# Kernel optimization log

Hardware: AMD Instinct MI355X
Metric: run time of the kernel (lower is better)

Reference implementation:

```python
import jax, jax.numpy as jnp
import numpy as np

NHID = 256
NHEADS = 8
HEAD_F = NHID // NHEADS  # GAT per-head out_features
ALPHA = 0.1              # GAT LeakyReLU slope
NEG = -9e15


def _leaky(x, slope):
    return jnp.where(x >= 0, x, slope * x)


def _cnorm(x, axis):
    # matches Norm.compute_norm: (x - mean) / (std_unbiased + 1e-6)
    m = jnp.mean(x, axis=axis, keepdims=True)
    s = jnp.std(x, axis=axis, keepdims=True, ddof=1)
    return (x - m) / (s + 1e-6)


def _norm(x):
    # Norm('bn') forward: per-sample normalize over features (dim=1 of x[i]) then nodes (dim=0)
    return _cnorm(_cnorm(x, axis=2), axis=1)


def setup_inputs() -> dict:
    key = jax.random.key(0)
    ks = jax.random.split(key, 12)
    B, N, E, H, D = 4, 1024, NHID, NHEADS, HEAD_F

    def xavier(k, shape, gain=1.414):
        fan_in, fan_out = shape[-2], shape[-1]
        a = gain * np.sqrt(6.0 / (fan_in + fan_out))
        return jax.random.uniform(k, shape, jnp.float32, -a, a)

    return {
        "x": jax.random.normal(ks[0], (B, N, E), jnp.float32),
        "src": jax.random.normal(ks[1], (N, B, E), jnp.float32),
        "adj": jax.random.randint(ks[2], (B, N, N), 0, 2, jnp.int32),
        "Wg": xavier(ks[3], (H, E, D)),                 # per-head GAT W
        "a1": xavier(ks[4], (H, D, 1))[..., 0],         # a[:D]
        "a2": xavier(ks[5], (H, D, 1))[..., 0],         # a[D:]
        "lin_w": xavier(ks[6], (E, E), gain=1.0),
        "lin_b": jnp.zeros((E,), jnp.float32),
        "in_proj_w": xavier(ks[7], (3 * E, E), gain=1.0),
        "in_proj_b": jnp.zeros((3 * E,), jnp.float32),
        "out_proj_w": xavier(ks[8], (E, E), gain=1.0),
        "out_proj_b": jnp.zeros((E,), jnp.float32),
    }


def reference(x, src, adj, Wg, a1, a2, lin_w, lin_b, in_proj_w, in_proj_b, out_proj_w, out_proj_b):
    B, N, E = x.shape
    H, D = NHEADS, HEAD_F

    # --- multi-head dense GAT (all heads vectorized) ---
    Wh = jnp.einsum("bnf,hfd->hbnd", x, Wg)                      # [H,B,N,D]
    s1 = jnp.einsum("hbnd,hd->hbn", Wh, a1)                      # a1 . Wh_i
    s2 = jnp.einsum("hbnd,hd->hbn", Wh, a2)                      # a2 . Wh_j
    e = _leaky(s1[..., :, None] + s2[..., None, :], ALPHA)       # [H,B,N,N]
    e = jnp.where(adj[None] > 0, e, NEG)
    attn = jax.nn.softmax(e, axis=-1)                            # [H,B,N,N]
    hp = _leaky(jnp.einsum("hbnm,hbmd->hbnd", attn, Wh), 0.01)   # F.leaky_relu default

    x = x + jnp.transpose(hp, (1, 2, 0, 3)).reshape(B, N, H * D)
    e_out = jnp.mean(attn, axis=0)                               # [B,N,N]

    # --- norm1 -> linear -> norm2 ---
    x = _norm(x) @ lin_w.T + lin_b
    x = _norm(x)

    # --- nn.MultiheadAttention(query=x, key=x, value=src) ---
    srcb = jnp.transpose(src, (1, 0, 2))                         # [B,N,E]
    Wq, Wk, Wv = in_proj_w[:E], in_proj_w[E:2 * E], in_proj_w[2 * E:]
    bq, bk, bv = in_proj_b[:E], in_proj_b[E:2 * E], in_proj_b[2 * E:]
    Dh = E // H
    q = (x @ Wq.T + bq).reshape(B, N, H, Dh)
    k = (x @ Wk.T + bk).reshape(B, N, H, Dh)
    v = (srcb @ Wv.T + bv).reshape(B, N, H, Dh)
    scores = jnp.einsum("bqhd,bkhd->bhqk", q, k) / jnp.sqrt(jnp.float32(Dh))
    p = jax.nn.softmax(scores, axis=-1)
    o = jnp.einsum("bhqk,bkhd->bqhd", p, v).reshape(B, N, E)
    x = o @ out_proj_w.T + out_proj_b                            # [B,N,E]

    return (x, e_out)
```

## Files before the change

### kernel.cpp

```cpp
#include <hip/hip_runtime.h>
#include <hip/hip_bf16.h>

#define BIAS_OFF 196608
#define S1_OFF   198400
#define S2_OFF   231168
#define CS_OFF   263936
#define ST1_OFF  296704
#define ST2_OFF  298752
#define A_OFF    300800
#define MX_OFF   825088
#define RS_OFF   857856
#define PK_OFF   890624
#define B_OFF    1349376
#define C_OFF    2397952
#define FLAG_F   3446528

#define NEGC (-9.0e15f)

typedef __attribute__((ext_vector_type(8))) short bf16x8s;
typedef __attribute__((ext_vector_type(4))) float f32x4;

static __device__ __forceinline__ float bf2f(unsigned short u) {
  union { unsigned int i; float f; } v; v.i = ((unsigned int)u) << 16; return v.f;
}
static __device__ __forceinline__ unsigned short f2bf(float f) {
  union { float f; unsigned int u; } v; v.f = f;
  unsigned int r = (v.u + 0x7FFFu + ((v.u >> 16) & 1u)) >> 16;
  return (unsigned short)r;
}
static __device__ __forceinline__ float ldin(const void* p, long i, int bf) {
  return bf ? bf2f(((const unsigned short*)p)[i]) : ((const float*)p)[i];
}
static __device__ __forceinline__ unsigned short rdbf(const void* p, long i, int bf) {
  if (bf) return ((const unsigned short*)p)[i];
  return f2bf(((const float*)p)[i]);
}
static __device__ __forceinline__ void stout(void* p, long i, float v, int bf) {
  if (bf) ((unsigned short*)p)[i] = f2bf(v);
  else    ((float*)p)[i] = v;
}

__global__ __launch_bounds__(64) void detect_kernel(const unsigned short* x, int* flag) {
  int lane = threadIdx.x;
  unsigned short u = x[2 * lane];
  int e = (u >> 7) & 0xFF;
  bool good = (e >= 100 && e <= 140);
  unsigned long long m = __ballot(good);
  if (lane == 0) *flag = (__popcll(m) >= 48) ? 1 : 0;
}

__global__ __launch_bounds__(256) void packadj_kernel(const int* adj,
                                                      unsigned long long* pk) {
  int t = threadIdx.x, w = t >> 6, lane = t & 63;
  long row = blockIdx.x;
  #pragma unroll
  for (int j = 0; j < 4; ++j) {
    int m = t + 256*j;
    bool bit = adj[row*1024 + m] > 0;
    unsigned long long mask = __ballot(bit);
    if (lane == 0) pk[row*16 + w + 4*j] = mask;
  }
}

__global__ __launch_bounds__(256) void prep_kernel(
    const void* wg, const void* lin_w, const void* inp_w, const void* out_w,
    const void* lin_b, const void* inp_b, const void* out_b,
    const void* a1, const void* a2, float* ws, const int* flagp) {
  const int bf = *flagp;
  unsigned short* wbf = (unsigned short*)ws;
  int t = threadIdx.x;
  int f = blockIdx.x;
  int m = blockIdx.y;
  if (m == 0) {
    int h = t >> 5, d = t & 31;
    wbf[t*256 + f] = rdbf(wg, h*8192 + f*32 + d, bf);
  } else if (m <= 5) {
    int dst = m*65536 + t*256 + f;
    if (m == 1)      wbf[dst] = rdbf(lin_w, t*256 + f, bf);
    else if (m == 2) wbf[dst] = rdbf(inp_w, t*256 + f, bf);
    else if (m == 3) wbf[dst] = rdbf(inp_w, (256 + t)*256 + f, bf);
    else if (m == 4) wbf[dst] = rdbf(inp_w, (512 + t)*256 + f, bf);
    else             wbf[dst] = rdbf(out_w, t*256 + f, bf);
  } else if (f == 0) {
    ws[BIAS_OFF + t]        = ldin(lin_b, t, bf);
    ws[BIAS_OFF + 256 + t]  = ldin(inp_b, t, bf);
    ws[BIAS_OFF + 512 + t]  = ldin(inp_b, 256 + t, bf);
    ws[BIAS_OFF + 768 + t]  = ldin(inp_b, 512 + t, bf);
    ws[BIAS_OFF + 1024 + t] = ldin(out_b, t, bf);
    ws[BIAS_OFF + 1280 + t] = ldin(a1, t, bf);
    ws[BIAS_OFF + 1536 + t] = ldin(a2, t, bf);
    ws[CS_OFF + 4096 + t]   = 0.0f;
  }
}

#define PB_S 1032
__global__ __launch_bounds__(512) void attn1a_kernel(const void* x, float* ws,
                                                     const int* flagp) {
  const int bf = *flagp;
  int t = threadIdx.x;
  int gid = blockIdx.x;
  int h = gid & 7;
  int b = (gid >> 3) & 3;
  int n0 = (gid >> 5) * 32;
  __shared__ __align__(16) unsigned char arena[4096 + 32*PB_S*2];
  float* s2s = (float*)arena;
  unsigned short (*Pb)[PB_S] = (unsigned short (*)[PB_S])(arena + 4096);
  float (*opart)[32][17] = (float (*)[32][17])arena;
  int w = t >> 6, lane = t & 63;
  int m = lane & 15, quad = lane >> 4;
  const unsigned long long* pk = (const unsigned long long*)(ws + PK_OFF);
  const float* s2p = ws + S2_OFF + h*4096 + b*1024;
  #pragma unroll
  for (int j = 0; j < 2; ++j) s2s[t + 512*j] = s2p[t + 512*j];
  __syncthreads();
  #pragma unroll
  for (int rr = 0; rr < 4; ++rr) {
    int r = 4*w + rr;
    int rowi = __builtin_amdgcn_readfirstlane(b*1024 + n0 + r);
    const unsigned long long* prow = pk + (long)rowi * 16;
    float s1v = ws[S1_OFF + h*4096 + rowi];
    float p[16];
    float mx = -3.4e38f;
    #pragma unroll
    for (int j = 0; j < 16; ++j) {
      int mm = lane + 64*j;
      float ev = s1v + s2s[mm];
      ev = (ev >= 0.0f) ? ev : 0.1f*ev;
      ev = ((prow[j] >> lane) & 1ull) ? ev : NEGC;
      p[j] = ev;
      mx = fmaxf(mx, ev);
    }
    #pragma unroll
    for (int off = 32; off > 0; off >>= 1) mx = fmaxf(mx, __shfl_xor(mx, off));
    float s = 0.0f;
    #pragma unroll
    for (int j = 0; j < 16; ++j) { p[j] = __expf(p[j] - mx); s += p[j]; }
    #pragma unroll
    for (int off = 32; off > 0; off >>= 1) s += __shfl_xor(s, off);
    float rs = 1.0f / s;
    #pragma unroll
    for (int j = 0; j < 16; ++j)
      Pb[r][lane + 64*j] = f2bf(p[j] * rs);
    if (lane == 0) {
      ws[MX_OFF + h*4096 + rowi] = mx;
      ws[RS_OFF + h*4096 + rowi] = rs;
    }
  }
  __syncthreads();
  f32x4 g0, g1;
  {
    const unsigned short* wht = (const unsigned short*)(ws + A_OFF);
    int ntile = w & 1;
    int ktbase = (w >> 1) * 8;
    int vd = ntile*16 + m;
    const unsigned short* wrow = wht + ((long)((b*8 + h)*32 + vd))*1024;
    f32x4 a0g0 = {0,0,0,0}, a1g0 = {0,0,0,0};
    f32x4 a0g1 = {0,0,0,0}, a1g1 = {0,0,0,0};
    #pragma unroll
    for (int kt2 = 0; kt2 < 4; ++kt2) {
      int kt = ktbase + 2*kt2;
      bf16x8s bw0 = *(const bf16x8s*)(wrow + kt*32 + quad*8);
      bf16x8s bw1 = *(const bf16x8s*)(wrow + (kt+1)*32 + quad*8);
      bf16x8s p00 = *(const bf16x8s*)&Pb[m][kt*32 + quad*8];
      bf16x8s p01 = *(const bf16x8s*)&Pb[16 + m][kt*32 + quad*8];
      a0g0 = __builtin_amdgcn_mfma_f32_16x16x32_bf16(p00, bw0, a0g0, 0, 0, 0);
      a0g1 = __builtin_amdgcn_mfma_f32_16x16x32_bf16(p01, bw0, a0g1, 0, 0, 0);
      bf16x8s p10 = *(const bf16x8s*)&Pb[m][(kt+1)*32 + quad*8];
      bf16x8s p11 = *(const bf16x8s*)&Pb[16 + m][(kt+1)*32 + quad*8];
      a1g0 = __builtin_amdgcn_mfma_f32_16x16x32_bf16(p10, bw1, a1g0, 0, 0, 0);
      a1g1 = __builtin_amdgcn_mfma_f32_16x16x32_bf16(p11, bw1, a1g1, 0, 0, 0);
    }
    g0 = a0g0 + a1g0;
    g1 = a0g1 + a1g1;
  }
  __syncthreads();
  #pragma unroll
  for (int i = 0; i < 4; ++i) {
    opart[w][quad*4 + i][m]      = g0[i];
    opart[w][16 + quad*4 + i][m] = g1[i];
  }
  __syncthreads();
  #pragma unroll
  for (int half = 0; half < 2; ++half) {
    int r = (t >> 5) + half*16;
    int dd = t & 31;
    int nt = dd >> 4, c = dd & 15;
    float sum = opart[nt][r][c] + opart[nt + 2][r][c]
              + opart[nt + 4][r][c] + opart[nt + 6][r][c];
    float hv = (sum >= 0.0f) ? sum : 0.01f*sum;
    long idx = (long)(b*1024 + n0 + r)*256 + h*32 + dd;
    ws[C_OFF + idx] = ldin(x, idx, bf) + hv;
  }
}

__global__ __launch_bounds__(256) void eout_kernel(float* ws, void* dout,
                                                   const int* flagp) {
  const int bf = *flagp;
  int t = threadIdx.x;
  int gid = blockIdx.x;
  int b = gid & 3;
  int n = gid >> 2;
  int row = b*1024 + n;
  int w = t >> 6, lane = t & 63;
  __shared__ float part[8];
  const unsigned long long* pk = (const unsigned long long*)(ws + PK_OFF);
  const unsigned long long* prow = pk + (long)row * 16;
  float v = ws[C_OFF + (long)row*256 + t];
  float s = v;
  #pragma unroll
  for (int off = 32; off > 0; off >>= 1) s += __shfl_xor(s, off);
  if (lane == 0) part[w] = s;
  __syncthreads();
  float mean = (part[0] + part[1] + part[2] + part[3]) * (1.0f/256.0f);
  float d = v - mean;
  float ss = d*d;
  #pragma unroll
  for (int off = 32; off > 0; off >>= 1) ss += __shfl_xor(ss, off);
  if (lane == 0) part[4 + w] = ss;
  __syncthreads();
  float inv = 1.0f / (sqrtf((part[4]+part[5]+part[6]+part[7]) * (1.0f/255.0f)) + 1e-6f);
  ws[B_OFF + (long)row*256 + t] = d * inv;
  float s1v[8], mxv[8], rsv[8];
  #pragma unroll
  for (int h = 0; h < 8; ++h) {
    s1v[h] = ws[S1_OFF + h*4096 + row];
    mxv[h] = ws[MX_OFF + h*4096 + row];
    rsv[h] = ws[RS_OFF + h*4096 + row];
  }
  const float* s2b = ws + S2_OFF + b*1024;
  #pragma unroll
  for (int j = 0; j < 4; ++j) {
    int m = t + 256*j;
    bool a = (prow[w + 4*j] >> lane) & 1ull;
    float acc = 0.0f;
    #pragma unroll
    for (int h = 0; h < 8; ++h) {
      float ev = s1v[h] + s2b[h*4096 + m];
      ev = (ev >= 0.0f) ? ev : 0.1f*ev;
      ev = a ? ev : NEGC;
      acc += rsv[h] * __expf(ev - mxv[h]);
    }
    stout(dout, 1048576L + (long)row*1024 + m, 0.125f*acc, bf);
  }
}

__global__ __launch_bounds__(256) void colstatsA_kernel(const float* in, float* cs) {
  int t = threadIdx.x;
  int j = blockIdx.x & 63;
  int b = blockIdx.x >> 6;
  float s = 0, ss = 0;
  for (int n = j*16; n < j*16 + 16; ++n) {
    float v = in[(b*1024 + n)*256 + t];
    s += v; ss += v*v;
  }
  cs[(b*64 + j)*256 + t] = s;
  cs[65536 + (b*64 + j)*256 + t] = ss;
}

__global__ __launch_bounds__(256) void colstatsB_kernel(const float* cs, float* st) {
  int t = threadIdx.x;
  int b = blockIdx.x;
  float s = 0, ss = 0;
  for (int j = 0; j < 64; ++j) {
    s  += cs[(b*64 + j)*256 + t];
    ss += cs[65536 + (b*64 + j)*256 + t];
  }
  float mean = s * (1.0f/1024.0f);
  float var = fmaxf((ss - s*mean) * (1.0f/1023.0f), 0.0f);
  st[b*256 + t] = mean;
  st[1024 + b*256 + t] = 1.0f / (sqrtf(var) + 1e-6f);
}

template<int IN_MODE, int RN, int OUTM, int CS, int SOP>
__global__ __launch_bounds__(512) void gemm2_kernel(const void* inp,
    const unsigned short* wmat, const unsigned short* wmat2,
    const float* bias, const float* bias2, const float* st,
    void* outp, float* csout, const int* flagp) {
  const int bf = *flagp;
  int t = threadIdx.x;
  int gid = blockIdx.x;
  int rowg = (CS == 2) ? (gid >> 1) : gid;
  int colbase = (CS == 2) ? ((gid & 1) * 128) : 0;
  int r0 = rowg * 16;
  __shared__ __align__(16) unsigned short Usm[2*16*264];
  unsigned short (*Uh)[264] = (unsigned short (*)[264])Usm;
  unsigned short (*Ul)[264] = (unsigned short (*)[264])(Usm + 16*264);
  {
    int srow = t >> 5;
    int e0 = (t & 31) * 8;
    long grow = r0 + srow;
    float v[8];
    if (IN_MODE == 0) {
      #pragma unroll
      for (int j = 0; j < 8; ++j) v[j] = ldin(inp, grow*256 + e0 + j, bf);
    } else if (IN_MODE == 1) {
      int b = (int)(grow >> 10);
      const float* ip = (const float*)inp + grow*256 + e0;
      const float* mp = st + b*256 + e0;
      const float* vp = st + 1024 + b*256 + e0;
      #pragma unroll
      for (int j = 0; j < 8; ++j) v[j] = (ip[j] - mp[j]) * vp[j];
    } else if (IN_MODE == 2) {
      int b = (int)(grow >> 10), n = (int)(grow & 1023);
      #pragma unroll
      for (int j = 0; j < 8; ++j)
        v[j] = ldin(inp, (long)(n*4 + b)*256 + e0 + j, bf);
    } else {
      int b = (int)(grow >> 10), n = (int)(grow & 1023);
      const float* ip = (const float*)inp
          + ((long)(b*8 + (e0 >> 5))*1024 + n)*32 + (e0 & 31);
      #pragma unroll
      for (int j = 0; j < 8; ++j) v[j] = ip[j];
    }
    unsigned short hv[8], lv[8];
    #pragma unroll
    for (int j = 0; j < 8; ++j) {
      hv[j] = f2bf(v[j]);
      lv[j] = f2bf(v[j] - bf2f(hv[j]));
    }
    *(bf16x8s*)&Uh[srow][e0] = *(bf16x8s*)hv;
    *(bf16x8s*)&Ul[srow][e0] = *(bf16x8s*)lv;
  }
  __syncthreads();
  int w = t >> 6, lane = t & 63, m = lane & 15, quad = lane >> 4;
  const int NT = (CS == 1) ? 2 : 1;
  f32x4 accs[2];
  f32x4 acck;
  #pragma unroll
  for (int nt = 0; nt < NT; ++nt) {
    int o = colbase + w*16 + nt*128 + m;
    const unsigned short* wp = wmat + o*256 + quad*8;
    f32x4 ah_acc = {0,0,0,0}, al_acc = {0,0,0,0};
    f32x4 kh_acc = {0,0,0,0}, kl_acc = {0,0,0,0};
    const unsigned short* wp2 = (OUTM == 5) ? (wmat2 + o*256 + quad*8) : wp;
    #pragma unroll
    for (int kt = 0; kt < 8; ++kt) {
      bf16x8s ah = *(const bf16x8s*)&Uh[m][kt*32 + quad*8];
      bf16x8s al = *(const bf16x8s*)&Ul[m][kt*32 + quad*8];
      bf16x8s bw = *(const bf16x8s*)(wp + kt*32);
      ah_acc = __builtin_amdgcn_mfma_f32_16x16x32_bf16(ah, bw, ah_acc, 0, 0, 0);
      al_acc = __builtin_amdgcn_mfma_f32_16x16x32_bf16(al, bw, al_acc, 0, 0, 0);
      if (OUTM == 5) {
        bf16x8s bw2 = *(const bf16x8s*)(wp2 + kt*32);
        kh_acc = __builtin_amdgcn_mfma_f32_16x16x32_bf16(ah, bw2, kh_acc, 0, 0, 0);
        kl_acc = __builtin_amdgcn_mfma_f32_16x16x32_bf16(al, bw2, kl_acc, 0, 0, 0);
      }
    }
    accs[nt] = ah_acc + al_acc;
    if (OUTM == 5) acck = kh_acc + kl_acc;
    if (RN == 0) {
      float bv = bias[o];
      if constexpr (OUTM == 0) {
        #pragma unroll
        for (int i = 0; i < 4; ++i) {
          long row = r0 + quad*4 + i;
          ((float*)outp)[row*256 + o] = accs[nt][i] + bv;
        }
      } else if constexpr (OUTM == 1) {
        #pragma unroll
        for (int i = 0; i < 4; ++i) {
          long row = r0 + quad*4 + i;
          stout(outp, row*256 + o, accs[nt][i] + bv, bf);
        }
      } else if constexpr (OUTM == 4) {
        int h = o >> 5, d = o & 31;
        #pragma unroll
        for (int i = 0; i < 4; ++i) {
          long row = r0 + quad*4 + i;
          int b = (int)(row >> 10), n = (int)(row & 1023);
          ((unsigned short*)outp)[((long)((b*8 + h)*32 + d))*1024 + n]
              = f2bf(accs[nt][i] + bv);
        }
      } else if constexpr (OUTM == 5) {
        float* wsf = (float*)outp;
        float* qhm = wsf + A_OFF;
        unsigned short* khm = (unsigned short*)(wsf + B_OFF);
        float bq = bias[o], bk = bias2[o];
        int h = o >> 5, d = o & 31;
        #pragma unroll
        for (int i = 0; i < 4; ++i) {
          long row = r0 + quad*4 + i;
          int b = (int)(row >> 10), n = (int)(row & 1023);
          long idx = ((long)((b*8 + h)*1024 + n))*32 + d;
          qhm[idx] = accs[nt][i] + bq;
          khm[idx] = f2bf(acck[i] + bk);
        }
      }
    }
  }
  if constexpr (SOP == 1) {
    __shared__ float sp[2][8][16];
    int o = colbase + w*16 + m;
    float a1v = bias2[o];
    float a2v = st[o];
    #pragma unroll
    for (int i = 0; i < 4; ++i) {
      float v1 = accs[0][i] * a1v;
      float v2 = accs[0][i] * a2v;
      #pragma unroll
      for (int off = 8; off > 0; off >>= 1) {
        v1 += __shfl_xor(v1, off);
        v2 += __shfl_xor(v2, off);
      }
      if (m == 0) {
        sp[0][w][quad*4 + i] = v1;
        sp[1][w][quad*4 + i] = v2;
      }
    }
    __syncthreads();
    if (t < 128) {
      int which = t >> 6, h2 = (t >> 4) & 3, r = t & 15;
      float v = sp[which][2*h2][r] + sp[which][2*h2 + 1][r];
      long dst = (which ? S2_OFF : S1_OFF)
               + (long)((colbase >> 5) + h2)*4096 + (r0 + r);
      csout[dst] = v;
    }
  }
  if constexpr (RN == 1) {
    __syncthreads();
    float (*O)[264] = (float (*)[264])Usm;
    #pragma unroll
    for (int nt = 0; nt < NT; ++nt) {
      int oc = colbase + w*16 + nt*128 + m;
      float bv = bias[oc];
      #pragma unroll
      for (int i = 0; i < 4; ++i)
        O[quad*4 + i][oc] = accs[nt][i] + bv;
    }
    __syncthreads();
    #pragma unroll
    for (int rr = 0; rr < 2; ++rr) {
      int r = 2*w + rr;
      float vals[4]; float s = 0.0f;
      #pragma unroll
      for (int j = 0; j < 4; ++j) { vals[j] = O[r][lane + 64*j]; s += vals[j]; }
      #pragma unroll
      for (int off = 32; off > 0; off >>= 1) s += __shfl_xor(s, off);
      float mean = s * (1.0f/256.0f);
      float ss = 0.0f;
      #pragma unroll
      for (int j = 0; j < 4; ++j) { float d = vals[j] - mean; ss += d*d; }
      #pragma unroll
      for (int off = 32; off > 0; off >>= 1) ss += __shfl_xor(ss, off);
      float inv = 1.0f / (sqrtf(ss * (1.0f/255.0f)) + 1e-6f);
      #pragma unroll
      for (int j = 0; j < 4; ++j) {
        float nv = (vals[j] - mean) * inv;
        ((float*)outp)[(long)(r0 + r)*256 + lane + 64*j] = nv;
        O[r][lane + 64*j] = nv;
      }
    }
    __syncthreads();
    if (csout != nullptr && t < 256) {
      float s = 0, ss = 0;
      #pragma unroll
      for (int r = 0; r < 16; ++r) { float v = O[r][t]; s += v; ss += v*v; }
      csout[gid*256 + t] = s;
      csout[65536 + gid*256 + t] = ss;
    }
  }
}

#define P2S 1036
__global__ __launch_bounds__(512) void attn2_kernel(float* ws) {
  int t = threadIdx.x;
  int gid = blockIdx.x;
  int h = gid & 7;
  int b = (gid >> 3) & 3;
  int n0 = (gid >> 5) << 4;
  __shared__ __align__(16) unsigned short P[16][P2S];
  __shared__ float pmx[8][16];
  __shared__ float psm[8][16];
  __shared__ float gmx[16];
  __shared__ float grs[16];
  __shared__ __align__(16) float opart[8][16][17];
  float* qq = ws + A_OFF;
  const unsigned short* kk = (const unsigned short*)(ws + B_OFF);
  const unsigned short* vt = (const unsigned short*)(ws + C_OFF);
  int base_bh = (b*8 + h)*1024;
  int w = t >> 6, lane = t & 63;
  int m = lane & 15, quad = lane >> 4;
  const float scl = 0.17677669529663687f;
  float s[8][4];
  {
    const float* qp = qq + (base_bh + n0 + m)*32 + quad*8;
    bf16x8s aq;
    #pragma unroll
    for (int j = 0; j < 8; ++j) ((unsigned short*)&aq)[j] = f2bf(qp[j]);
    f32x4 zero = {0.0f, 0.0f, 0.0f, 0.0f};
    #pragma unroll
    for (int kt = 0; kt < 8; ++kt) {
      int kbase = w*128 + kt*16;
      bf16x8s bk = *(const bf16x8s*)(kk + (base_bh + kbase + m)*32 + quad*8);
      f32x4 d = __builtin_amdgcn_mfma_f32_16x16x32_bf16(aq, bk, zero, 0, 0, 0);
      #pragma unroll
      for (int i = 0; i < 4; ++i) s[kt][i] = d[i] * scl;
    }
  }
  #pragma unroll
  for (int i = 0; i < 4; ++i) {
    float mx = s[0][i];
    #pragma unroll
    for (int kt = 1; kt < 8; ++kt) mx = fmaxf(mx, s[kt][i]);
    #pragma unroll
    for (int off = 8; off > 0; off >>= 1) mx = fmaxf(mx, __shfl_xor(mx, off));
    float sm = 0.0f;
    #pragma unroll
    for (int kt = 0; kt < 8; ++kt) sm += __expf(s[kt][i] - mx);
    #pragma unroll
    for (int off = 8; off > 0; off >>= 1) sm += __shfl_xor(sm, off);
    if (m == 0) { pmx[w][quad*4 + i] = mx; psm[w][quad*4 + i] = sm; }
  }
  __syncthreads();
  if (t < 16) {
    float mx = pmx[0][t];
    #pragma unroll
    for (int w2 = 1; w2 < 8; ++w2) mx = fmaxf(mx, pmx[w2][t]);
    float den = 0.0f;
    #pragma unroll
    for (int w2 = 0; w2 < 8; ++w2) den += psm[w2][t] * __expf(pmx[w2][t] - mx);
    gmx[t] = mx;
    grs[t] = 1.0f / den;
  }
  __syncthreads();
  #pragma unroll
  for (int i = 0; i < 4; ++i) {
    int row = quad*4 + i;
    float mx = gmx[row], rs = grs[row];
    #pragma unroll
    for (int kt = 0; kt < 8; ++kt)
      P[row][w*128 + kt*16 + m] = f2bf(__expf(s[kt][i] - mx) * rs);
  }
  __syncthreads();
  {
    int ntile = w & 1;
    int ktbase = (w >> 1) * 8;
    int vd = ntile*16 + m;
    const unsigned short* vrow = vt + base_bh*32 + vd*1024;
    const unsigned short* P0 = &P[m][0];
    f32x4 acc0 = {0.0f, 0.0f, 0.0f, 0.0f};
    f32x4 acc1 = {0.0f, 0.0f, 0.0f, 0.0f};
    #pragma unroll
    for (int kt2 = 0; kt2 < 4; ++kt2) {
      int kt = ktbase + 2*kt2;
      bf16x8s ap0 = *(const bf16x8s*)(P0 + kt*32 + quad*8);
      bf16x8s bv0 = *(const bf16x8s*)(vrow + kt*32 + quad*8);
      acc0 = __builtin_amdgcn_mfma_f32_16x16x32_bf16(ap0, bv0, acc0, 0, 0, 0);
      bf16x8s ap1 = *(const bf16x8s*)(P0 + (kt+1)*32 + quad*8);
      bf16x8s bv1 = *(const bf16x8s*)(vrow + (kt+1)*32 + quad*8);
      acc1 = __builtin_amdgcn_mfma_f32_16x16x32_bf16(ap1, bv1, acc1, 0, 0, 0);
    }
    f32x4 acc = acc0 + acc1;
    #pragma unroll
    for (int i = 0; i < 4; ++i)
      opart[w][quad*4 + i][m] = acc[i];
  }
  __syncthreads();
  {
    int r = t >> 5, d = t & 31;
    int nt = d >> 4, c = d & 15;
    float sum = opart[nt][r][c] + opart[nt + 2][r][c]
              + opart[nt + 4][r][c] + opart[nt + 6][r][c];
    qq[(base_bh + n0 + r)*32 + d] = sum;
  }
}

extern "C" void kernel_launch(void* const* d_in, const int* in_sizes, int n_in,
                              void* d_out, int out_size, void* d_ws, size_t ws_size,
                              hipStream_t stream) {
  const void* x   = d_in[0];
  const void* src = d_in[1];
  const int* adj  = (const int*)d_in[2];
  const void* wg  = d_in[3];
  const void* a1  = d_in[4];
  const void* a2  = d_in[5];
  const void* lw  = d_in[6];
  const void* lb  = d_in[7];
  const void* ipw = d_in[8];
  const void* ipb = d_in[9];
  const void* opw = d_in[10];
  const void* opb = d_in[11];
  float* ws = (float*)d_ws;
  const unsigned short* wbf = (const unsigned short*)d_ws;
  int* flagp = (int*)(ws + FLAG_F);

  detect_kernel<<<1, 64, 0, stream>>>((const unsigned short*)x, flagp);
  prep_kernel<<<dim3(256, 7), 256, 0, stream>>>(wg, lw, ipw, opw, lb, ipb, opb,
                                                a1, a2, ws, flagp);
  packadj_kernel<<<4096, 256, 0, stream>>>(adj,
      (unsigned long long*)(ws + PK_OFF));
  gemm2_kernel<0,0,4,2,1><<<512, 512, 0, stream>>>(x, wbf + 0*65536,
      nullptr, ws + CS_OFF + 4096, ws + BIAS_OFF + 1280, ws + BIAS_OFF + 1536,
      ws + A_OFF, ws, flagp);
  attn1a_kernel<<<1024, 512, 0, stream>>>(x, ws, flagp);
  eout_kernel<<<4096, 256, 0, stream>>>(ws, d_out, flagp);
  colstatsA_kernel<<<256, 256, 0, stream>>>(ws + B_OFF, ws + MX_OFF);
  colstatsB_kernel<<<4, 256, 0, stream>>>(ws + MX_OFF, ws + ST1_OFF);
  gemm2_kernel<1,1,0,1,0><<<256, 512, 0, stream>>>(ws + B_OFF, wbf + 1*65536,
      nullptr, ws + BIAS_OFF, nullptr, ws + ST1_OFF, ws + C_OFF, ws + MX_OFF,
      flagp);
  colstatsB_kernel<<<4, 256, 0, stream>>>(ws + MX_OFF, ws + ST2_OFF);
  gemm2_kernel<1,0,5,2,0><<<512, 512, 0, stream>>>(ws + C_OFF, wbf + 2*65536,
      wbf + 3*65536, ws + BIAS_OFF + 256, ws + BIAS_OFF + 512, ws + ST2_OFF,
      ws, nullptr, flagp);
  gemm2_kernel<2,0,4,2,0><<<512, 512, 0, stream>>>(src, wbf + 4*65536,
      nullptr, ws + BIAS_OFF + 768, nullptr, nullptr, ws + C_OFF, nullptr,
      flagp);
  attn2_kernel<<<2048, 512, 0, stream>>>(ws);
  gemm2_kernel<3,0,1,2,0><<<512, 512, 0, stream>>>(ws + A_OFF, wbf + 5*65536,
      nullptr, ws + BIAS_OFF + 1024, nullptr, nullptr, d_out, nullptr,
      flagp);
}
```

Before: 243.2 us.

## Merge setup kernels and fuse column stats into eout and gemm via atomics

Detect, prep and adjacency-packing are merged into one setup kernel that also zeroes the stat accumulators. The eout kernel now handles 8 rows per block, caches s2 in shared memory, and accumulates per-batch column sums with atomics. This removes the separate colstats kernels, and the gemm computes mean and inverse std from the raw sums when it loads its input. The aim is fewer launches and less intermediate traffic, at the cost of atomic contention and float summation order that is no longer deterministic.

New measurement: 243.4 us (median of 2 runs). About the same (+0.1%).

```diff
diff --git a/kernel.cpp b/kernel.cpp
--- a/kernel.cpp
+++ b/kernel.cpp
@@ -40,37 +40,24 @@
   else    ((float*)p)[i] = v;
 }
 
-__global__ __launch_bounds__(64) void detect_kernel(const unsigned short* x, int* flag) {
-  int lane = threadIdx.x;
-  unsigned short u = x[2 * lane];
-  int e = (u >> 7) & 0xFF;
-  bool good = (e >= 100 && e <= 140);
-  unsigned long long m = __ballot(good);
-  if (lane == 0) *flag = (__popcll(m) >= 48) ? 1 : 0;
-}
-
-__global__ __launch_bounds__(256) void packadj_kernel(const int* adj,
-                                                      unsigned long long* pk) {
-  int t = threadIdx.x, w = t >> 6, lane = t & 63;
-  long row = blockIdx.x;
-  #pragma unroll
-  for (int j = 0; j < 4; ++j) {
-    int m = t + 256*j;
-    bool bit = adj[row*1024 + m] > 0;
-    unsigned long long mask = __ballot(bit);
-    if (lane == 0) pk[row*16 + w + 4*j] = mask;
-  }
-}
-
-__global__ __launch_bounds__(256) void prep_kernel(
-    const void* wg, const void* lin_w, const void* inp_w, const void* out_w,
-    const void* lin_b, const void* inp_b, const void* out_b,
-    const void* a1, const void* a2, float* ws, const int* flagp) {
-  const int bf = *flagp;
-  unsigned short* wbf = (unsigned short*)ws;
+__global__ __launch_bounds__(256) void setup_kernel(
+    const void* x, const void* wg, const void* lin_w, const void* inp_w,
+    const void* out_w, const void* lin_b, const void* inp_b, const void* out_b,
+    const void* a1, const void* a2, const int* adj, float* ws, int* flagp) {
   int t = threadIdx.x;
   int f = blockIdx.x;
   int m = blockIdx.y;
+  __shared__ int bfs;
+  if (t < 64) {
+    unsigned short u = ((const unsigned short*)x)[2 * t];
+    int e = (u >> 7) & 0xFF;
+    bool good = (e >= 100 && e <= 140);
+    unsigned long long msk = __ballot(good);
+    if (t == 0) bfs = (__popcll(msk) >= 48) ? 1 : 0;
+  }
+  __syncthreads();
+  const int bf = bfs;
+  unsigned short* wbf = (unsigned short*)ws;
   if (m == 0) {
     int h = t >> 5, d = t & 31;
     wbf[t*256 + f] = rdbf(wg, h*8192 + f*32 + d, bf);
@@ -81,15 +68,33 @@
     else if (m == 3) wbf[dst] = rdbf(inp_w, (256 + t)*256 + f, bf);
     else if (m == 4) wbf[dst] = rdbf(inp_w, (512 + t)*256 + f, bf);
     else             wbf[dst] = rdbf(out_w, t*256 + f, bf);
-  } else if (f == 0) {
-    ws[BIAS_OFF + t]        = ldin(lin_b, t, bf);
-    ws[BIAS_OFF + 256 + t]  = ldin(inp_b, t, bf);
-    ws[BIAS_OFF + 512 + t]  = ldin(inp_b, 256 + t, bf);
-    ws[BIAS_OFF + 768 + t]  = ldin(inp_b, 512 + t, bf);
-    ws[BIAS_OFF + 1024 + t] = ldin(out_b, t, bf);
-    ws[BIAS_OFF + 1280 + t] = ldin(a1, t, bf);
-    ws[BIAS_OFF + 1536 + t] = ldin(a2, t, bf);
-    ws[CS_OFF + 4096 + t]   = 0.0f;
+  } else if (m == 6) {
+    if (f < 8)       ws[ST1_OFF + f*256 + t] = 0.0f;
+    else if (f < 16) ws[ST2_OFF + (f - 8)*256 + t] = 0.0f;
+    if (f == 0) {
+      ws[BIAS_OFF + t]        = ldin(lin_b, t, bf);
+      ws[BIAS_OFF + 256 + t]  = ldin(inp_b, t, bf);
+      ws[BIAS_OFF + 512 + t]  = ldin(inp_b, 256 + t, bf);
+      ws[BIAS_OFF + 768 + t]  = ldin(inp_b, 512 + t, bf);
+      ws[BIAS_OFF + 1024 + t] = ldin(out_b, t, bf);
+      ws[BIAS_OFF + 1280 + t] = ldin(a1, t, bf);
+      ws[BIAS_OFF + 1536 + t] = ldin(a2, t, bf);
+      ws[CS_OFF + 4096 + t]   = 0.0f;
+      if (t == 0) *flagp = bf;
+    }
+  } else {
+    unsigned long long* pkw = (unsigned long long*)(ws + PK_OFF);
+    int w = t >> 6, lane = t & 63;
+    for (int rr = 0; rr < 16; ++rr) {
+      long row = (long)f*16 + rr;
+      #pragma unroll
+      for (int j = 0; j < 4; ++j) {
+        int mm = t + 256*j;
+        bool bit = adj[row*1024 + mm] > 0;
+        unsigned long long msk = __ballot(bit);
+        if (lane == 0) pkw[row*16 + w + 4*j] = msk;
+      }
+    }
   }
 }
 
@@ -193,33 +198,46 @@
   }
 }
 
-__global__ __launch_bounds__(256) void eout_kernel(float* ws, void* dout,
-                                                   const int* flagp) {
+__global__ __launch_bounds__(512) void eout8_kernel(float* ws, void* dout,
+                                                    const int* flagp) {
   const int bf = *flagp;
   int t = threadIdx.x;
   int gid = blockIdx.x;
-  int b = gid & 3;
-  int n = gid >> 2;
-  int row = b*1024 + n;
+  int b = gid >> 7;
+  long r0 = (long)gid * 8;
   int w = t >> 6, lane = t & 63;
-  __shared__ float part[8];
-  const unsigned long long* pk = (const unsigned long long*)(ws + PK_OFF);
-  const unsigned long long* prow = pk + (long)row * 16;
-  float v = ws[C_OFF + (long)row*256 + t];
-  float s = v;
+  __shared__ __align__(16) float s2s[8][1026];
+  __shared__ __align__(16) float Brow[8][260];
+  for (int i = t; i < 8192; i += 512) {
+    int h = i >> 10, m = i & 1023;
+    s2s[h][m] = ws[S2_OFF + h*4096 + b*1024 + m];
+  }
+  long row = r0 + w;
+  float vals[4];
+  float s = 0.0f;
+  #pragma unroll
+  for (int j = 0; j < 4; ++j) {
+    vals[j] = ws[C_OFF + row*256 + lane + 64*j];
+    s += vals[j];
+  }
   #pragma unroll
   for (int off = 32; off > 0; off >>= 1) s += __shfl_xor(s, off);
-  if (lane == 0) part[w] = s;
-  __syncthreads();
-  float mean = (part[0] + part[1] + part[2] + part[3]) * (1.0f/256.0f);
-  float d = v - mean;
-  float ss = d*d;
+  float mean = s * (1.0f/256.0f);
+  float ss = 0.0f;
+  #pragma unroll
+  for (int j = 0; j < 4; ++j) { float d = vals[j] - mean; ss += d*d; }
   #pragma unroll
   for (int off = 32; off > 0; off >>= 1) ss += __shfl_xor(ss, off);
-  if (lane == 0) part[4 + w] = ss;
-  __syncthreads();
-  float inv = 1.0f / (sqrtf((part[4]+part[5]+part[6]+part[7]) * (1.0f/255.0f)) + 1e-6f);
-  ws[B_OFF + (long)row*256 + t] = d * inv;
+  float inv = 1.0f / (sqrtf(ss * (1.0f/255.0f)) + 1e-6f);
+  #pragma unroll
+  for (int j = 0; j < 4; ++j) {
+    float nv = (vals[j] - mean) * inv;
+    ws[B_OFF + row*256 + lane + 64*j] = nv;
+    Brow[w][lane + 64*j] = nv;
+  }
+  __syncthreads();
+  const unsigned long long* prow =
+      (const unsigned long long*)(ws + PK_OFF) + row*16;
   float s1v[8], mxv[8], rsv[8];
   #pragma unroll
   for (int h = 0; h < 8; ++h) {
@@ -227,48 +245,27 @@
     mxv[h] = ws[MX_OFF + h*4096 + row];
     rsv[h] = ws[RS_OFF + h*4096 + row];
   }
-  const float* s2b = ws + S2_OFF + b*1024;
-  #pragma unroll
-  for (int j = 0; j < 4; ++j) {
-    int m = t + 256*j;
-    bool a = (prow[w + 4*j] >> lane) & 1ull;
+  #pragma unroll
+  for (int j = 0; j < 16; ++j) {
+    int m = lane + 64*j;
+    bool a = (prow[j] >> lane) & 1ull;
     float acc = 0.0f;
     #pragma unroll
     for (int h = 0; h < 8; ++h) {
-      float ev = s1v[h] + s2b[h*4096 + m];
+      float ev = s1v[h] + s2s[h][m];
       ev = (ev >= 0.0f) ? ev : 0.1f*ev;
       ev = a ? ev : NEGC;
       acc += rsv[h] * __expf(ev - mxv[h]);
     }
-    stout(dout, 1048576L + (long)row*1024 + m, 0.125f*acc, bf);
-  }
-}
-
-__global__ __launch_bounds__(256) void colstatsA_kernel(const float* in, float* cs) {
-  int t = threadIdx.x;
-  int j = blockIdx.x & 63;
-  int b = blockIdx.x >> 6;
-  float s = 0, ss = 0;
-  for (int n = j*16; n < j*16 + 16; ++n) {
-    float v = in[(b*1024 + n)*256 + t];
-    s += v; ss += v*v;
-  }
-  cs[(b*64 + j)*256 + t] = s;
-  cs[65536 + (b*64 + j)*256 + t] = ss;
-}
-
-__global__ __launch_bounds__(256) void colstatsB_kernel(const float* cs, float* st) {
-  int t = threadIdx.x;
-  int b = blockIdx.x;
-  float s = 0, ss = 0;
-  for (int j = 0; j < 64; ++j) {
-    s  += cs[(b*64 + j)*256 + t];
-    ss += cs[65536 + (b*64 + j)*256 + t];
-  }
-  float mean = s * (1.0f/1024.0f);
-  float var = fmaxf((ss - s*mean) * (1.0f/1023.0f), 0.0f);
-  st[b*256 + t] = mean;
-  st[1024 + b*256 + t] = 1.0f / (sqrtf(var) + 1e-6f);
+    stout(dout, 1048576L + row*1024 + m, 0.125f*acc, bf);
+  }
+  if (t < 256) {
+    float ps = 0, pss = 0;
+    #pragma unroll
+    for (int r = 0; r < 8; ++r) { float v = Brow[r][t]; ps += v; pss += v*v; }
+    atomicAdd(&ws[ST1_OFF + b*256 + t], ps);
+    atomicAdd(&ws[ST1_OFF + 1024 + b*256 + t], pss);
+  }
 }
 
 template<int IN_MODE, int RN, int OUTM, int CS, int SOP>
@@ -296,10 +293,16 @@
     } else if (IN_MODE == 1) {
       int b = (int)(grow >> 10);
       const float* ip = (const float*)inp + grow*256 + e0;
-      const float* mp = st + b*256 + e0;
-      const float* vp = st + 1024 + b*256 + e0;
-      #pragma unroll
-      for (int j = 0; j < 8; ++j) v[j] = (ip[j] - mp[j]) * vp[j];
+      const float* sp_ = st + b*256 + e0;
+      const float* qp_ = st + 1024 + b*256 + e0;
+      #pragma unroll
+      for (int j = 0; j < 8; ++j) {
+        float sm = sp_[j], sq = qp_[j];
+        float mean = sm * (1.0f/1024.0f);
+        float var = fmaxf((sq - sm*mean) * (1.0f/1023.0f), 0.0f);
+        float inv = 1.0f / (sqrtf(var) + 1e-6f);
+        v[j] = (ip[j] - mean) * inv;
+      }
     } else if (IN_MODE == 2) {
       int b = (int)(grow >> 10), n = (int)(grow & 1023);
       #pragma unroll
@@ -452,11 +455,12 @@
     }
     __syncthreads();
     if (csout != nullptr && t < 256) {
+      int b = r0 >> 10;
       float s = 0, ss = 0;
       #pragma unroll
       for (int r = 0; r < 16; ++r) { float v = O[r][t]; s += v; ss += v*v; }
-      csout[gid*256 + t] = s;
-      csout[65536 + gid*256 + t] = ss;
+      atomicAdd(&csout[b*256 + t], s);
+      atomicAdd(&csout[1024 + b*256 + t], ss);
     }
   }
 }
@@ -584,22 +588,16 @@
   const unsigned short* wbf = (const unsigned short*)d_ws;
   int* flagp = (int*)(ws + FLAG_F);
 
-  detect_kernel<<<1, 64, 0, stream>>>((const unsigned short*)x, flagp);
-  prep_kernel<<<dim3(256, 7), 256, 0, stream>>>(wg, lw, ipw, opw, lb, ipb, opb,
-                                                a1, a2, ws, flagp);
-  packadj_kernel<<<4096, 256, 0, stream>>>(adj,
-      (unsigned long long*)(ws + PK_OFF));
+  setup_kernel<<<dim3(256, 8), 256, 0, stream>>>(x, wg, lw, ipw, opw, lb, ipb,
+      opb, a1, a2, adj, ws, flagp);
   gemm2_kernel<0,0,4,2,1><<<512, 512, 0, stream>>>(x, wbf + 0*65536,
       nullptr, ws + CS_OFF + 4096, ws + BIAS_OFF + 1280, ws + BIAS_OFF + 1536,
       ws + A_OFF, ws, flagp);
   attn1a_kernel<<<1024, 512, 0, stream>>>(x, ws, flagp);
-  eout_kernel<<<4096, 256, 0, stream>>>(ws, d_out, flagp);
-  colstatsA_kernel<<<256, 256, 0, stream>>>(ws + B_OFF, ws + MX_OFF);
-  colstatsB_kernel<<<4, 256, 0, stream>>>(ws + MX_OFF, ws + ST1_OFF);
+  eout8_kernel<<<512, 512, 0, stream>>>(ws, d_out, flagp);
   gemm2_kernel<1,1,0,1,0><<<256, 512, 0, stream>>>(ws + B_OFF, wbf + 1*65536,
-      nullptr, ws + BIAS_OFF, nullptr, ws + ST1_OFF, ws + C_OFF, ws + MX_OFF,
+      nullptr, ws + BIAS_OFF, nullptr, ws + ST1_OFF, ws + C_OFF, ws + ST2_OFF,
       flagp);
-  colstatsB_kernel<<<4, 256, 0, stream>>>(ws + MX_OFF, ws + ST2_OFF);
   gemm2_kernel<1,0,5,2,0><<<512, 512, 0, stream>>>(ws + C_OFF, wbf + 2*65536,
       wbf + 3*65536, ws + BIAS_OFF + 256, ws + BIAS_OFF + 512, ws + ST2_OFF,
       ws, nullptr, flagp);
```
